# Kernel tuning notes

Measured on AMD Instinct MI355X. Metric: run time of the kernel, lower is better.

Reference implementation:

```python
import jax, jax.numpy as jnp
import numpy as np

G = 8        # GroupNorm groups
PAD = 2      # kernel 5 -> same padding
TOPK = 2
TEMP = 1.0
EPS_GN = 1e-5

def conv1d(x, w):
    # x: (B,C,T), w: (Cout,Cin,K)
    return jax.lax.conv_general_dilated(x, w, (1,), [(PAD, PAD)],
                                        dimension_numbers=('NCH', 'OIH', 'NCH'))

def group_norm(x, g, b):
    B, C, T = x.shape
    xg = x.reshape(B, G, C // G, T)
    m = xg.mean((2, 3), keepdims=True)
    v = xg.var((2, 3), keepdims=True)
    xn = ((xg - m) * jax.lax.rsqrt(v + EPS_GN)).reshape(B, C, T)
    return xn * g[None, :, None] + b[None, :, None]

def gelu(x):
    return jax.nn.gelu(x, approximate=False)  # torch nn.GELU default (erf)

def layer_norm(x, g, b):
    m = x.mean(-1, keepdims=True)
    v = x.var(-1, keepdims=True)
    return (x - m) * jax.lax.rsqrt(v + EPS_GN) * g + b

def cnn_block(x, W1, g1, b1, W2, g2, b2, W3, g3, b3):
    # conv -> GN -> GELU, 3 layers, channel doubling (dropout=eval identity)
    h = gelu(group_norm(conv1d(x, W1), g1, b1))
    h = gelu(group_norm(conv1d(h, W2), g2, b2))
    h = gelu(group_norm(conv1d(h, W3), g3, b3))
    return h

def setup_inputs() -> dict:
    key = jax.random.key(0)
    ks = iter(jax.random.split(key, 64))
    def rn(shape, s):
        return jax.random.normal(next(ks), shape, jnp.float32) * s
    B, Cin, T = 64, 16, 512
    E, c1, c2, c3 = 8, 64, 128, 256
    Hrt, Drt, H, NC = 128, 64, 256, 10
    d = {}
    d['x'] = jax.random.normal(next(ks), (B, Cin, T), jnp.float32)
    # stacked expert CNN params (E leading axis)
    d['eW1'] = rn((E, c1, Cin, 5), 0.1); d['eg1'] = jnp.ones((E, c1)); d['eb1'] = jnp.zeros((E, c1))
    d['eW2'] = rn((E, c2, c1, 5), 0.05); d['eg2'] = jnp.ones((E, c2)); d['eb2'] = jnp.zeros((E, c2))
    d['eW3'] = rn((E, c3, c2, 5), 0.04); d['eg3'] = jnp.ones((E, c3)); d['eb3'] = jnp.zeros((E, c3))
    # shared (always-on) expert CNN
    d['sW1'] = rn((c1, Cin, 5), 0.1); d['sg1'] = jnp.ones((c1,)); d['sb1'] = jnp.zeros((c1,))
    d['sW2'] = rn((c2, c1, 5), 0.05); d['sg2'] = jnp.ones((c2,)); d['sb2'] = jnp.zeros((c2,))
    d['sW3'] = rn((c3, c2, 5), 0.04); d['sg3'] = jnp.ones((c3,)); d['sb3'] = jnp.zeros((c3,))
    # ContextProjRouter: conv front-end -> GAP -> 2-layer MLP
    d['rW'] = rn((Hrt, Cin, 5), 0.1); d['rg'] = jnp.ones((Hrt,)); d['rb'] = jnp.zeros((Hrt,))
    d['rm1W'] = rn((Hrt, Hrt), 0.08); d['rm1b'] = jnp.zeros((Hrt,))
    d['rlng'] = jnp.ones((Hrt,)); d['rlnb'] = jnp.zeros((Hrt,))
    d['rm2W'] = rn((Hrt, Drt), 0.08); d['rm2b'] = jnp.zeros((Drt,))
    # MOEGate linear
    d['gW'] = rn((Drt, E), 0.1); d['gb'] = jnp.zeros((E,))
    # LSTM (single layer, torch gate order i,f,g,o; forget bias = 1)
    d['W_ih'] = rn((c3, 4 * H), 0.04)
    d['W_hh'] = rn((H, 4 * H), 0.04)
    bl = np.zeros(4 * H, np.float32); bl[H:2 * H] = 1.0
    d['b_lstm'] = jnp.asarray(bl)
    # classifier head
    d['Wc'] = rn((H, NC), 0.05); d['bc'] = jnp.zeros((NC,))
    return d

def reference(x, eW1, eg1, eb1, eW2, eg2, eb2, eW3, eg3, eb3,
              sW1, sg1, sb1, sW2, sg2, sb2, sW3, sg3, sb3,
              rW, rg, rb, rm1W, rm1b, rlng, rlnb, rm2W, rm2b,
              gW, gb, W_ih, W_hh, b_lstm, Wc, bc):
    B = x.shape[0]
    # --- expert branches (vmapped over E) -> (E,B,256,T) ---
    expert_out = jax.vmap(
        lambda W1, g1, b1, W2, g2, b2, W3, g3, b3:
            cnn_block(x, W1, g1, b1, W2, g2, b2, W3, g3, b3)
    )(eW1, eg1, eb1, eW2, eg2, eb2, eW3, eg3, eb3)
    # --- shared expert (always on) ---
    shared = cnn_block(x, sW1, sg1, sb1, sW2, sg2, sb2, sW3, sg3, sb3)
    # --- router: conv -> GN -> GELU -> GAP -> MLP ---
    rh = gelu(group_norm(conv1d(x, rW), rg, rb)).mean(-1)      # (B,128)
    r = gelu(layer_norm(rh @ rm1W + rm1b, rlng, rlnb)) @ rm2W + rm2b  # (B,64)
    # --- MOEGate: softmax -> top-k mask -> renormalize ---
    w_soft = jax.nn.softmax((r @ gW + gb) / TEMP, axis=-1)     # (B,E)
    _, idx = jax.lax.top_k(w_soft, TOPK)                       # (B,K)
    mask = jnp.zeros_like(w_soft).at[jnp.arange(B)[:, None], idx].set(1.0)
    w_hard = w_soft * mask
    w_hard = w_hard / (w_hard.sum(-1, keepdims=True) + 1e-9)
    # --- weighted expert mixture + shared ---
    h = shared + jnp.einsum('be,ebct->bct', w_hard, expert_out)  # (B,256,T)
    # --- LSTM over time, take last hidden state ---
    H = W_hh.shape[0]
    seq = h.transpose(2, 0, 1)  # (T,B,256)
    def step(carry, xt):
        hh, cc = carry
        gates = xt @ W_ih + hh @ W_hh + b_lstm
        i, f, g, o = jnp.split(gates, 4, axis=-1)
        cc = jax.nn.sigmoid(f) * cc + jax.nn.sigmoid(i) * jnp.tanh(g)
        hh = jax.nn.sigmoid(o) * jnp.tanh(cc)
        return (hh, cc), None
    init = (jnp.zeros((B, H), x.dtype), jnp.zeros((B, H), x.dtype))
    (hT, _), _ = jax.lax.scan(step, init, seq)
    return hT @ Wc + bc  # (B,num_classes)
```

## Files before the change

kernel.cpp:

```cpp
#include <hip/hip_runtime.h>
#include <cstdint>
#include <cstddef>


#define DEVI __device__ __forceinline__

typedef _Float16 f16;
typedef _Float16 f16x8 __attribute__((ext_vector_type(8)));
typedef _Float16 f16x2 __attribute__((ext_vector_type(2)));
typedef float    f32x4 __attribute__((ext_vector_type(4)));
typedef unsigned int u32;
typedef unsigned short u16;

static constexpr int B   = 64;
static constexpr int T   = 512;
static constexpr int NC  = 10;
static constexpr int NU  = 192;

constexpr size_t SZ_WS1 = (size_t)5*64*32*2;
constexpr size_t SZ_WS2 = (size_t)5*128*64*2;
constexpr size_t SZ_WS3 = (size_t)5*256*128*2;
constexpr size_t SZ_WE1 = 8*SZ_WS1;
constexpr size_t SZ_WE2 = 8*SZ_WS2;
constexpr size_t SZ_WE3 = 8*SZ_WS3;
constexpr size_t SZ_WR  = (size_t)5*128*32*2;
constexpr size_t SZ_WIH = (size_t)1024*256*2;
constexpr size_t SZ_WHH = (size_t)128*1024*4;
constexpr size_t SZ_ACT0 = (size_t)B*T*32*2;
constexpr size_t SZ_RACT = (size_t)B*T*128*2;
constexpr size_t SZ_AMIX = (size_t)B*T*256*2;
constexpr size_t SZ_CONV = (size_t)NU*T*256*2;
constexpr size_t SZ_A1   = (size_t)NU*T*64*2;
constexpr size_t SZ_A2   = (size_t)NU*T*128*2;
constexpr size_t SZ_U    = (size_t)B*T*1024*2;
constexpr size_t SZ_STAT = (size_t)NU*8*2*4;
constexpr size_t SZ_STATR= (size_t)B*8*2*4;
constexpr size_t SZ_RH   = (size_t)B*128*4;
constexpr size_t SZ_EIDX = (size_t)B*2*4;
constexpr size_t SZ_SWT  = (size_t)B*2*4;
constexpr size_t SZ_HT   = (size_t)B*256*4;

constexpr size_t OFF_WS1  = 0;
constexpr size_t OFF_WS2  = OFF_WS1 + SZ_WS1;
constexpr size_t OFF_WS3  = OFF_WS2 + SZ_WS2;
constexpr size_t OFF_WE1  = OFF_WS3 + SZ_WS3;
constexpr size_t OFF_WE2  = OFF_WE1 + SZ_WE1;
constexpr size_t OFF_WE3  = OFF_WE2 + SZ_WE2;
constexpr size_t OFF_WR   = OFF_WE3 + SZ_WE3;
constexpr size_t OFF_WIH  = OFF_WR  + SZ_WR;
constexpr size_t OFF_WHH  = OFF_WIH + SZ_WIH;
constexpr size_t OFF_ACT0 = OFF_WHH + SZ_WHH;
constexpr size_t OFF_RACT = OFF_ACT0 + SZ_ACT0;
constexpr size_t OFF_AMIX = OFF_RACT + SZ_RACT;
constexpr size_t OFF_CONV = OFF_AMIX + SZ_AMIX;
constexpr size_t OFF_A1   = OFF_CONV + SZ_CONV;
constexpr size_t OFF_A2   = OFF_A1 + SZ_A1;
constexpr size_t OFF_U    = OFF_CONV;
constexpr size_t OFF_STAT = OFF_A2 + SZ_A2;
constexpr size_t OFF_STATR= OFF_STAT + SZ_STAT;
constexpr size_t OFF_RH   = OFF_STATR + SZ_STATR;
constexpr size_t OFF_EIDX = OFF_RH + SZ_RH;
constexpr size_t OFF_SWT  = OFF_EIDX + SZ_EIDX;
constexpr size_t OFF_HT   = OFF_SWT + SZ_SWT;
constexpr size_t WS_TOTAL = OFF_HT + SZ_HT;

static_assert(SZ_U <= SZ_CONV + SZ_A1 + SZ_A2, "U alias overflow");

DEVI float geluf(float x){ return 0.5f*x*(1.f + erff(x*0.70710678118654752f)); }
DEVI float fsig(float x){ return 1.f/(1.f + __expf(-x)); }
DEVI float ftanh(float x){ float e = __expf(-2.f*x); return (1.f-e)/(1.f+e); }

DEVI void fill_convw(f16* dst, const float* src, int COUT, int CI, int CIP, int idx){
  int s  = idx / (COUT*CIP);
  int r  = idx - s*(COUT*CIP);
  int co = r / CIP;
  int ci = r - co*CIP;
  float v = (ci < CI) ? src[((size_t)co*CI + ci)*5 + s] : 0.f;
  dst[idx] = (f16)v;
}

__global__ __launch_bounds__(256) void k_prep_w(
    const float* eW1, const float* eW2, const float* eW3,
    const float* sW1, const float* sW2, const float* sW3, const float* rW,
    const float* Wih, const float* Whh, char* ws)
{
  int i = blockIdx.x*256 + threadIdx.x;
  if (i < 10240){ fill_convw((f16*)(ws+OFF_WS1), sW1, 64, 16, 32, i); return; } i -= 10240;
  if (i < 40960){ fill_convw((f16*)(ws+OFF_WS2), sW2, 128, 64, 64, i); return; } i -= 40960;
  if (i < 163840){ fill_convw((f16*)(ws+OFF_WS3), sW3, 256, 128, 128, i); return; } i -= 163840;
  if (i < 81920){ int e=i/10240, r=i-e*10240;
    fill_convw((f16*)(ws+OFF_WE1)+ (size_t)e*10240, eW1 + (size_t)e*64*16*5, 64, 16, 32, r); return; } i -= 81920;
  if (i < 327680){ int e=i/40960, r=i-e*40960;
    fill_convw((f16*)(ws+OFF_WE2)+ (size_t)e*40960, eW2 + (size_t)e*128*64*5, 128, 64, 64, r); return; } i -= 327680;
  if (i < 1310720){ int e=i/163840, r=i-e*163840;
    fill_convw((f16*)(ws+OFF_WE3)+ (size_t)e*163840, eW3 + (size_t)e*163840, 256, 128, 128, r); return; } i -= 1310720;
  if (i < 20480){ fill_convw((f16*)(ws+OFF_WR), rW, 128, 16, 32, i); return; } i -= 20480;
  if (i < 262144){
    int j = i >> 8, k = i & 255;
    ((f16*)(ws+OFF_WIH))[i] = (f16)Wih[(size_t)k*1024 + j]; return; } i -= 262144;
  if (i < 131072){
    int i2 = i >> 10, j = i & 1023;
    f16 a = (f16)Whh[(size_t)(2*i2)*1024 + j];
    f16 b = (f16)Whh[(size_t)(2*i2+1)*1024 + j];
    u32 u = (u32)__builtin_bit_cast(unsigned short, a)
          | ((u32)__builtin_bit_cast(unsigned short, b) << 16);
    ((u32*)(ws+OFF_WHH))[i] = u; return; }
}

__global__ __launch_bounds__(256) void k_prep_x(const float* __restrict__ x, char* ws){
  int idx = blockIdx.x*256 + threadIdx.x;
  if (idx >= B*T*32) return;
  int b = idx/(T*32); int r = idx - b*(T*32); int t = r >> 5; int c = r & 31;
  f16 v = (c < 16) ? (f16)x[((size_t)b*16 + c)*T + t] : (f16)0.f;
  ((f16*)(ws+OFF_ACT0))[idx] = v;
}

template<int CIN, int NSHIFT>
__global__ __launch_bounds__(256) void k_conv(
    const f16* __restrict__ act, long actUnitStride,
    const f16* __restrict__ wtS, const f16* __restrict__ wtE, long wtEStride,
    const int* __restrict__ eidx,
    f16* __restrict__ outp, const float* __restrict__ bias, int COUT)
{
  int u = blockIdx.z;
  int s = u >> 6, b = u & 63;
  const f16* wt = wtS;
  if (eidx && s < 2) wt = wtE + (size_t)eidx[b*2+s]*wtEStride;
  const f16* abase = act + (actUnitStride ? (size_t)u*actUnitStride
                                          : (size_t)b*T*CIN);
  f16* obase = outp + (size_t)u*T*COUT;

  int t0 = blockIdx.x << 6;
  int n0 = blockIdx.y << 6;
  int tid  = threadIdx.x;
  int wave = tid >> 6, lane = tid & 63;
  int lr = lane & 15, lk = lane >> 4;

  f32x4 acc[4];
  #pragma unroll
  for (int nf=0; nf<4; ++nf) acc[nf] = f32x4{0.f,0.f,0.f,0.f};

  int trow = t0 + wave*16 + lr;

  #pragma unroll
  for (int sh=0; sh<NSHIFT; ++sh){
    int tg = (NSHIFT==5) ? (trow + sh - 2) : trow;
    bool valid = (unsigned)tg < (unsigned)T;
    const f16* arow = abase + (long)tg*CIN + lk*8;
    #pragma unroll
    for (int c0=0; c0<CIN; c0+=32){
      f16x8 af = {(f16)0,(f16)0,(f16)0,(f16)0,(f16)0,(f16)0,(f16)0,(f16)0};
      if (valid) af = *(const f16x8*)(arow + c0);
      #pragma unroll
      for (int nf=0; nf<4; ++nf){
        int col = n0 + nf*16 + lr;
        f16x8 bf = *(const f16x8*)(wt + ((size_t)sh*COUT + col)*CIN + c0 + lk*8);
        acc[nf] = __builtin_amdgcn_mfma_f32_16x16x32_f16(af, bf, acc[nf], 0, 0, 0);
      }
    }
  }

  #pragma unroll
  for (int nf=0; nf<4; ++nf){
    int col = n0 + nf*16 + lr;
    float bv = bias ? bias[col] : 0.f;
    #pragma unroll
    for (int r=0; r<4; ++r){
      int trw = t0 + wave*16 + lk*4 + r;
      obase[(size_t)trw*COUT + col] = (f16)(acc[nf][r] + bv);
    }
  }
}

template<int CPG>
__global__ __launch_bounds__(256) void k_gnstats(
    const f16* __restrict__ xin, float* __restrict__ stats)
{
  constexpr int C = CPG*8;
  constexpr int V = CPG/8;
  int u = blockIdx.x >> 3, g = blockIdx.x & 7;
  const f16* base = xin + (size_t)u*T*C + g*CPG;
  float sum = 0.f, ss = 0.f;
  for (int i = threadIdx.x; i < T*V; i += 256){
    int t = i / V, v = i - (i/V)*V;
    f16x8 xv = *(const f16x8*)(base + (size_t)t*C + v*8);
    #pragma unroll
    for (int k=0;k<8;++k){ float f = (float)xv[k]; sum += f; ss += f*f; }
  }
  #pragma unroll
  for (int off=32; off; off>>=1){ sum += __shfl_down(sum, off); ss += __shfl_down(ss, off); }
  __shared__ float rs[8];
  int wave = threadIdx.x >> 6, lane = threadIdx.x & 63;
  if (lane == 0){ rs[wave] = sum; rs[4+wave] = ss; }
  __syncthreads();
  if (threadIdx.x == 0){
    float S = rs[0]+rs[1]+rs[2]+rs[3], Q = rs[4]+rs[5]+rs[6]+rs[7];
    constexpr float N = (float)(CPG*T);
    float m = S/N;
    float var = Q/N - m*m;
    stats[(u*8+g)*2]   = m;
    stats[(u*8+g)*2+1] = rsqrtf(var + 1e-5f);
  }
}

template<int CPG>
__global__ __launch_bounds__(256) void k_gnapply(
    const f16* __restrict__ xin, const float* __restrict__ stats,
    const float* __restrict__ gS, const float* __restrict__ bS,
    const float* __restrict__ gE, const float* __restrict__ bE,
    const int* __restrict__ eidx, f16* __restrict__ outp, int total8)
{
  constexpr int C = CPG*8;
  int idx = blockIdx.x*256 + threadIdx.x;
  if (idx >= total8) return;
  size_t base = (size_t)idx*8;
  int u = (int)(base / ((size_t)T*C));
  int s = u >> 6, b = u & 63;
  const float* gamma = gS; const float* beta = bS;
  if (eidx && s < 2){ int e = eidx[b*2+s]; gamma = gE + e*C; beta = bE + e*C; }
  int c0 = (int)(base % C);
  int g  = c0 / CPG;
  float m  = stats[(u*8+g)*2];
  float rstd = stats[(u*8+g)*2+1];
  f16x8 xv = *(const f16x8*)(xin + base);
  f16x8 h8;
  #pragma unroll
  for (int k=0; k<8; ++k){
    float xn = ((float)xv[k]-m)*rstd*gamma[c0+k] + beta[c0+k];
    h8[k] = (f16)geluf(xn);
  }
  *(f16x8*)(outp + base) = h8;
}

__global__ __launch_bounds__(256) void k_gnmix(
    const f16* __restrict__ conv, const float* __restrict__ stats,
    const float* __restrict__ sg, const float* __restrict__ sb,
    const float* __restrict__ eg, const float* __restrict__ eb,
    const int* __restrict__ eidx, const float* __restrict__ swt,
    f16* __restrict__ amix)
{
  size_t base = ((size_t)blockIdx.x*256 + threadIdx.x)*8;
  if (base >= (size_t)B*T*256) return;
  int b = (int)(base / ((size_t)T*256));
  size_t rem = base - (size_t)b*T*256;
  int c0 = (int)(rem & 255);
  int g  = c0 >> 5;
  float o[8] = {0.f,0.f,0.f,0.f,0.f,0.f,0.f,0.f};
  #pragma unroll
  for (int s=0; s<3; ++s){
    int u = s*64 + b;
    float w; const float *gamma, *beta;
    if (s < 2){ int e = eidx[b*2+s]; w = swt[b*2+s]; gamma = eg + e*256; beta = eb + e*256; }
    else      { w = 1.f; gamma = sg; beta = sb; }
    float m = stats[(u*8+g)*2], rstd = stats[(u*8+g)*2+1];
    f16x8 xv = *(const f16x8*)(conv + (size_t)u*T*256 + rem);
    #pragma unroll
    for (int k=0; k<8; ++k){
      float xn = ((float)xv[k]-m)*rstd*gamma[c0+k] + beta[c0+k];
      o[k] += w*geluf(xn);
    }
  }
  f16x8 h8;
  #pragma unroll
  for (int k=0; k<8; ++k) h8[k] = (f16)o[k];
  *(f16x8*)(amix + base) = h8;
}

__global__ __launch_bounds__(512) void k_gap(const f16* __restrict__ ract,
                                             float* __restrict__ rh){
  int b = blockIdx.x;
  int c = threadIdx.x & 127, st = threadIdx.x >> 7;
  const f16* p = ract + (size_t)b*T*128 + c;
  float s = 0.f;
  for (int t = st; t < T; t += 4) s += (float)p[(size_t)t*128];
  __shared__ float acc[512];
  acc[threadIdx.x] = s;
  __syncthreads();
  if (st == 0) rh[b*128 + c] = (acc[c] + acc[128+c] + acc[256+c] + acc[384+c]) * (1.f/(float)T);
}

__global__ __launch_bounds__(128) void k_router(
    const float* __restrict__ rh,
    const float* __restrict__ m1W, const float* __restrict__ m1b,
    const float* __restrict__ lng, const float* __restrict__ lnb,
    const float* __restrict__ m2W, const float* __restrict__ m2b,
    const float* __restrict__ gW,  const float* __restrict__ gb,
    int* __restrict__ eidx, float* __restrict__ swt)
{
  int b = blockIdx.x, j = threadIdx.x;
  __shared__ float sbuf[128];
  __shared__ float red[4];
  __shared__ float z2[64];
  sbuf[j] = rh[b*128 + j];
  __syncthreads();
  float acc = m1b[j];
  for (int k=0; k<128; ++k) acc += sbuf[k]*m1W[k*128 + j];
  float s1 = acc, s2 = acc*acc;
  #pragma unroll
  for (int off=32; off; off>>=1){ s1 += __shfl_down(s1, off); s2 += __shfl_down(s2, off); }
  int wid = j >> 6, lane = j & 63;
  if (lane == 0){ red[wid] = s1; red[2+wid] = s2; }
  __syncthreads();
  float S = red[0]+red[1], Q = red[2]+red[3];
  float m = S*(1.f/128.f), var = Q*(1.f/128.f) - m*m;
  float xn = (acc - m)*rsqrtf(var + 1e-5f)*lng[j] + lnb[j];
  float ge = geluf(xn);
  __syncthreads();
  sbuf[j] = ge;
  __syncthreads();
  if (j < 64){
    float a = m2b[j];
    for (int k=0; k<128; ++k) a += sbuf[k]*m2W[k*64 + j];
    z2[j] = a;
  }
  __syncthreads();
  if (j == 0){
    float lg[8];
    for (int e=0; e<8; ++e){
      float a = gb[e];
      for (int k=0; k<64; ++k) a += z2[k]*gW[k*8 + e];
      lg[e] = a;
    }
    float mx = lg[0];
    for (int e=1; e<8; ++e) mx = fmaxf(mx, lg[e]);
    float p[8], sum = 0.f;
    for (int e=0; e<8; ++e){ p[e] = __expf(lg[e]-mx); sum += p[e]; }
    float inv = 1.f/sum;
    for (int e=0; e<8; ++e) p[e] *= inv;
    int i1 = 0;
    for (int e=1; e<8; ++e) if (p[e] > p[i1]) i1 = e;
    int i2 = -1;
    for (int e=0; e<8; ++e){ if (e==i1) continue; if (i2 < 0 || p[e] > p[i2]) i2 = e; }
    float s = p[i1] + p[i2] + 1e-9f;
    eidx[b*2]   = i1;  swt[b*2]   = p[i1]/s;
    eidx[b*2+1] = i2;  swt[b*2+1] = p[i2]/s;
  }
}

constexpr int PV5 = 100;
constexpr int PLQ = 7;

DEVI float dot2acc(u32 wu, u32 hu, float acc){
#if __has_builtin(__builtin_amdgcn_fdot2)
  return __builtin_amdgcn_fdot2(__builtin_bit_cast(f16x2, wu),
                                __builtin_bit_cast(f16x2, hu), acc, false);
#else
  f16x2 a = __builtin_bit_cast(f16x2, wu), b = __builtin_bit_cast(f16x2, hu);
  return acc + (float)a.x*(float)b.x + (float)a.y*(float)b.y;
#endif
}

__global__ __attribute__((amdgpu_flat_work_group_size(512,512), amdgpu_waves_per_eu(2,2)))
void k_lstm(const u32* __restrict__ whh, const f16* __restrict__ U,
            float* __restrict__ hTout)
{
  int b = blockIdx.x, j = threadIdx.x;
  int d = j & 255, half = j >> 8;
  int colA = half*256 + d;
  int colB = 512 + colA;

  __shared__ u32 wl[PLQ*4*1024];
  __shared__ __align__(16) u32 hbuf[2][128];
  __shared__ float gbF[256], gbO[256];

  u32 wA[PV5], wB[PV5];
  #pragma unroll
  for (int i=0; i<PV5; ++i){
    wA[i] = whh[(size_t)i*1024 + colA];
    wB[i] = whh[(size_t)i*1024 + colB];
  }
  for (int idx = j; idx < PLQ*4*1024; idx += 512){
    int p = idx >> 10, c = idx & 1023;
    wl[idx] = whh[(size_t)(PV5+p)*1024 + c];
  }
  if (j < 128) hbuf[0][j] = 0u;

  float cst = 0.f, hst = 0.f;
  const f16* Ub = U + (size_t)b*T*1024;
  float uA = (float)Ub[colA], uB = (float)Ub[colB];
  __syncthreads();

  int cur = 0;
  for (int t=0; t<T; ++t){
    float aA = uA, aB = uB;
    if (t+1 < T){
      const f16* un = Ub + (size_t)(t+1)*1024;
      uA = (float)un[colA]; uB = (float)un[colB];
    }
    const uint4* hp4 = (const uint4*)hbuf[cur];
    #pragma unroll
    for (int q=0; q<PV5/4; ++q){
      uint4 hq = hp4[q];
      aA = dot2acc(wA[4*q+0], hq.x, aA); aB = dot2acc(wB[4*q+0], hq.x, aB);
      aA = dot2acc(wA[4*q+1], hq.y, aA); aB = dot2acc(wB[4*q+1], hq.y, aB);
      aA = dot2acc(wA[4*q+2], hq.z, aA); aB = dot2acc(wB[4*q+2], hq.z, aB);
      aA = dot2acc(wA[4*q+3], hq.w, aA); aB = dot2acc(wB[4*q+3], hq.w, aB);
    }
    #pragma unroll
    for (int k=0; k<PLQ; ++k){
      uint4 hq = hp4[PV5/4 + k];
      u32 a0 = wl[(4*k+0)*1024 + colA], b0 = wl[(4*k+0)*1024 + colB];
      u32 a1 = wl[(4*k+1)*1024 + colA], b1 = wl[(4*k+1)*1024 + colB];
      u32 a2 = wl[(4*k+2)*1024 + colA], b2 = wl[(4*k+2)*1024 + colB];
      u32 a3 = wl[(4*k+3)*1024 + colA], b3 = wl[(4*k+3)*1024 + colB];
      aA = dot2acc(a0, hq.x, aA); aB = dot2acc(b0, hq.x, aB);
      aA = dot2acc(a1, hq.y, aA); aB = dot2acc(b1, hq.y, aB);
      aA = dot2acc(a2, hq.z, aA); aB = dot2acc(b2, hq.z, aB);
      aA = dot2acc(a3, hq.w, aA); aB = dot2acc(b3, hq.w, aB);
    }
    if (half){ gbF[d] = aA; gbO[d] = aB; }
    __syncthreads();
    if (!half){
      float gi = aA, gg = aB, gf = gbF[d], go = gbO[d];
      cst = fsig(gf)*cst + fsig(gi)*ftanh(gg);
      hst = fsig(go)*ftanh(cst);
      u16* hn = (u16*)hbuf[cur^1];
      hn[d] = __builtin_bit_cast(u16, (f16)hst);
    }
    __syncthreads();
    cur ^= 1;
  }
  if (!half) hTout[b*256 + d] = hst;
}

__global__ __launch_bounds__(256) void k_head(const float* __restrict__ hT,
    const float* __restrict__ Wc, const float* __restrict__ bc,
    float* __restrict__ out)
{
  int b = blockIdx.x, j = threadIdx.x;
  __shared__ float hs[256];
  hs[j] = hT[b*256 + j];
  __syncthreads();
  if (j < NC){
    float a = bc[j];
    for (int k=0; k<256; ++k) a += hs[k]*Wc[k*NC + j];
    out[b*NC + j] = a;
  }
}

extern "C" void kernel_launch(void* const* d_in, const int* in_sizes, int n_in,
                              void* d_out, int out_size, void* d_ws, size_t ws_size,
                              hipStream_t stream)
{
  if (ws_size < WS_TOTAL) return;

  const float* x    = (const float*)d_in[0];
  const float* eW1  = (const float*)d_in[1];
  const float* eg1  = (const float*)d_in[2];
  const float* eb1  = (const float*)d_in[3];
  const float* eW2  = (const float*)d_in[4];
  const float* eg2  = (const float*)d_in[5];
  const float* eb2  = (const float*)d_in[6];
  const float* eW3  = (const float*)d_in[7];
  const float* eg3  = (const float*)d_in[8];
  const float* eb3  = (const float*)d_in[9];
  const float* sW1  = (const float*)d_in[10];
  const float* sg1  = (const float*)d_in[11];
  const float* sb1  = (const float*)d_in[12];
  const float* sW2  = (const float*)d_in[13];
  const float* sg2  = (const float*)d_in[14];
  const float* sb2  = (const float*)d_in[15];
  const float* sW3  = (const float*)d_in[16];
  const float* sg3  = (const float*)d_in[17];
  const float* sb3  = (const float*)d_in[18];
  const float* rW   = (const float*)d_in[19];
  const float* rg   = (const float*)d_in[20];
  const float* rb   = (const float*)d_in[21];
  const float* rm1W = (const float*)d_in[22];
  const float* rm1b = (const float*)d_in[23];
  const float* rlng = (const float*)d_in[24];
  const float* rlnb = (const float*)d_in[25];
  const float* rm2W = (const float*)d_in[26];
  const float* rm2b = (const float*)d_in[27];
  const float* gW   = (const float*)d_in[28];
  const float* gb   = (const float*)d_in[29];
  const float* Wih  = (const float*)d_in[30];
  const float* Whh  = (const float*)d_in[31];
  const float* blst = (const float*)d_in[32];
  const float* Wc   = (const float*)d_in[33];
  const float* bc   = (const float*)d_in[34];

  char* ws = (char*)d_ws;
  f16*  ws1   = (f16*)(ws + OFF_WS1);
  f16*  ws2   = (f16*)(ws + OFF_WS2);
  f16*  ws3   = (f16*)(ws + OFF_WS3);
  f16*  we1   = (f16*)(ws + OFF_WE1);
  f16*  we2   = (f16*)(ws + OFF_WE2);
  f16*  we3   = (f16*)(ws + OFF_WE3);
  f16*  wr    = (f16*)(ws + OFF_WR);
  f16*  wih   = (f16*)(ws + OFF_WIH);
  u32*  whh   = (u32*)(ws + OFF_WHH);
  f16*  act0  = (f16*)(ws + OFF_ACT0);
  f16*  ract  = (f16*)(ws + OFF_RACT);
  f16*  amix  = (f16*)(ws + OFF_AMIX);
  f16*  convb = (f16*)(ws + OFF_CONV);
  f16*  a1    = (f16*)(ws + OFF_A1);
  f16*  a2    = (f16*)(ws + OFF_A2);
  f16*  Ubuf  = (f16*)(ws + OFF_U);
  float* stats = (float*)(ws + OFF_STAT);
  float* statsR= (float*)(ws + OFF_STATR);
  float* rh    = (float*)(ws + OFF_RH);
  int*   eidx  = (int*)(ws + OFF_EIDX);
  float* swt   = (float*)(ws + OFF_SWT);
  float* hTb   = (float*)(ws + OFF_HT);

  k_prep_w<<<(2349056 + 255)/256, 256, 0, stream>>>(eW1,eW2,eW3,sW1,sW2,sW3,rW,Wih,Whh,ws);
  k_prep_x<<<(B*T*32 + 255)/256, 256, 0, stream>>>(x, ws);

  k_conv<32,5><<<dim3(8,2,64), 256, 0, stream>>>(act0, 0L, wr, nullptr, 0L, nullptr, convb, nullptr, 128);
  k_gnstats<16><<<64*8, 256, 0, stream>>>(convb, statsR);
  k_gnapply<16><<<2048, 256, 0, stream>>>(convb, statsR, rg, rb, nullptr, nullptr, nullptr, ract, 64*T*128/8);
  k_gap<<<B, 512, 0, stream>>>(ract, rh);
  k_router<<<B, 128, 0, stream>>>(rh, rm1W, rm1b, rlng, rlnb, rm2W, rm2b, gW, gb, eidx, swt);

  k_conv<32,5><<<dim3(8,1,NU), 256, 0, stream>>>(act0, 0L, ws1, we1, (long)(5*64*32), eidx, convb, nullptr, 64);
  k_gnstats<8><<<NU*8, 256, 0, stream>>>(convb, stats);
  k_gnapply<8><<<3072, 256, 0, stream>>>(convb, stats, sg1, sb1, eg1, eb1, eidx, a1, NU*T*64/8);

  k_conv<64,5><<<dim3(8,2,NU), 256, 0, stream>>>(a1, (long)T*64, ws2, we2, (long)(5*128*64), eidx, convb, nullptr, 128);
  k_gnstats<16><<<NU*8, 256, 0, stream>>>(convb, stats);
  k_gnapply<16><<<6144, 256, 0, stream>>>(convb, stats, sg2, sb2, eg2, eb2, eidx, a2, NU*T*128/8);

  k_conv<128,5><<<dim3(8,4,NU), 256, 0, stream>>>(a2, (long)T*128, ws3, we3, (long)(5*256*128), eidx, convb, nullptr, 256);
  k_gnstats<32><<<NU*8, 256, 0, stream>>>(convb, stats);
  k_gnmix<<<4096, 256, 0, stream>>>(convb, stats, sg3, sb3, eg3, eb3, eidx, swt, amix);

  k_conv<256,1><<<dim3(8,16,64), 256, 0, stream>>>(amix, 0L, wih, nullptr, 0L, nullptr, Ubuf, blst, 1024);
  k_lstm<<<B, 512, 0, stream>>>(whh, Ubuf, hTb);
  k_head<<<B, 256, 0, stream>>>(hTb, Wc, bc, (float*)d_out);
}
```

Before: 1.657 ms.

## Fuse conv, GroupNorm stats, apply and GELU into one per-unit layer kernel

Replaces the separate conv, GroupNorm-stats and GroupNorm-apply kernels with a single kernel per layer. Each block computes the full time extent of one unit's conv output into shared memory, reduces the group statistics there, and applies normalisation plus GELU before writing. For the router this also folds global average pooling into the same kernel. This removes the fp16 round trips of the conv output through global memory and several launches. The cost is far fewer blocks (192 or 384 per layer, 64 for the router) and heavy LDS use (up to 128 KB per block), which limits occupancy.

Result: slower. 1.773 ms (+7.0%).

```diff
diff --git a/kernel.cpp b/kernel.cpp
--- a/kernel.cpp
+++ b/kernel.cpp
@@ -115,6 +115,144 @@
   ((f16*)(ws+OFF_ACT0))[idx] = v;
 }
 
+template<int CIN, int COUT_BLK, int CPG, bool GAP>
+__global__ __launch_bounds__(512) void k_layer(
+    const f16* __restrict__ act, long actUnitStride,
+    const f16* __restrict__ wtS, const f16* __restrict__ wtE, long wtEStride,
+    const int* __restrict__ eidx,
+    const float* __restrict__ gS, const float* __restrict__ bS,
+    const float* __restrict__ gE, const float* __restrict__ bE,
+    int COUT_TOTAL,
+    f16* __restrict__ outp, long outUnitStride, int outStride,
+    float* __restrict__ rhOut)
+{
+  constexpr int CH8  = COUT_BLK/8;
+  constexpr int NG   = COUT_BLK/CPG;
+  constexpr int CPW  = CPG/8;
+  constexpr int NPASS = COUT_BLK/64;
+  constexpr int ROWSTEP = 512/CH8;
+  constexpr int ITERS   = T/ROWSTEP;
+
+  int u = blockIdx.x, hf = blockIdx.y;
+  int s_ = u >> 6, b = u & 63;
+  const f16* wt = wtS;
+  const float* gamma = gS; const float* beta = bS;
+  if (eidx && s_ < 2){
+    int e = eidx[b*2 + s_];
+    wt    = wtE + (size_t)e*wtEStride;
+    gamma = gE + (size_t)e*COUT_TOTAL;
+    beta  = bE + (size_t)e*COUT_TOTAL;
+  }
+  gamma += hf*COUT_BLK; beta += hf*COUT_BLK;
+  const f16* abase = act + (actUnitStride ? (size_t)u*actUnitStride
+                                          : (size_t)b*T*CIN);
+  int wcol0 = hf*COUT_BLK;
+
+  __shared__ f16 tile[T*COUT_BLK];
+  __shared__ float cpart[8][CH8][2];
+  __shared__ float mr[NG][2];
+  __shared__ float gcol[GAP ? 8 : 1][GAP ? CH8 : 1][8];
+
+  int tid = threadIdx.x;
+  int wave = tid >> 6, lane = tid & 63;
+  int lr = lane & 15, lk = lane >> 4;
+
+  for (int mt = wave; mt < 32; mt += 8){
+    int trow = mt*16 + lr;
+    #pragma unroll
+    for (int np = 0; np < NPASS; ++np){
+      f32x4 acc[4];
+      #pragma unroll
+      for (int nf=0; nf<4; ++nf) acc[nf] = f32x4{0.f,0.f,0.f,0.f};
+      #pragma unroll
+      for (int sh = 0; sh < 5; ++sh){
+        int tg = trow + sh - 2;
+        bool valid = (unsigned)tg < (unsigned)T;
+        const f16* arow = abase + (long)tg*CIN + lk*8;
+        #pragma unroll
+        for (int c0=0; c0<CIN; c0+=32){
+          f16x8 af = {(f16)0,(f16)0,(f16)0,(f16)0,(f16)0,(f16)0,(f16)0,(f16)0};
+          if (valid) af = *(const f16x8*)(arow + c0);
+          #pragma unroll
+          for (int nf=0; nf<4; ++nf){
+            int col = wcol0 + np*64 + nf*16 + lr;
+            f16x8 bf = *(const f16x8*)(wt + ((size_t)sh*COUT_TOTAL + col)*CIN + c0 + lk*8);
+            acc[nf] = __builtin_amdgcn_mfma_f32_16x16x32_f16(af, bf, acc[nf], 0, 0, 0);
+          }
+        }
+      }
+      #pragma unroll
+      for (int nf=0; nf<4; ++nf)
+        #pragma unroll
+        for (int r=0; r<4; ++r)
+          tile[(size_t)(mt*16 + lk*4 + r)*COUT_BLK + np*64 + nf*16 + lr] = (f16)acc[nf][r];
+    }
+  }
+  __syncthreads();
+
+  int chunk = tid & (CH8-1);
+  int row0  = tid / CH8;
+  float sum = 0.f, ss = 0.f;
+  #pragma unroll
+  for (int k=0; k<ITERS; ++k){
+    int row = row0 + k*ROWSTEP;
+    f16x8 xv = *(const f16x8*)(tile + (size_t)row*COUT_BLK + chunk*8);
+    #pragma unroll
+    for (int e=0;e<8;++e){ float f = (float)xv[e]; sum += f; ss += f*f; }
+  }
+  #pragma unroll
+  for (int mk=CH8; mk<=32; mk<<=1){ sum += __shfl_xor(sum, mk); ss += __shfl_xor(ss, mk); }
+  if (lane < CH8){ cpart[wave][lane][0] = sum; cpart[wave][lane][1] = ss; }
+  __syncthreads();
+  if (tid < NG){
+    float S = 0.f, Q = 0.f;
+    for (int w2=0; w2<8; ++w2)
+      for (int cc=0; cc<CPW; ++cc){ S += cpart[w2][tid*CPW+cc][0]; Q += cpart[w2][tid*CPW+cc][1]; }
+    constexpr float N = (float)(CPG*T);
+    float m = S/N, var = Q/N - m*m;
+    mr[tid][0] = m; mr[tid][1] = rsqrtf(var + 1e-5f);
+  }
+  __syncthreads();
+
+  int g = chunk / CPW;
+  float m = mr[g][0], rstd = mr[g][1];
+  float gm[8], bt[8];
+  #pragma unroll
+  for (int e=0;e<8;++e){ gm[e] = gamma[chunk*8+e]; bt[e] = beta[chunk*8+e]; }
+  float cs[8] = {0.f,0.f,0.f,0.f,0.f,0.f,0.f,0.f};
+  f16* obase = outp ? (outp + (size_t)u*outUnitStride + hf*COUT_BLK) : nullptr;
+  #pragma unroll
+  for (int k=0; k<ITERS; ++k){
+    int row = row0 + k*ROWSTEP;
+    f16x8 xv = *(const f16x8*)(tile + (size_t)row*COUT_BLK + chunk*8);
+    f16x8 h8;
+    #pragma unroll
+    for (int e=0;e<8;++e){
+      float xn = ((float)xv[e]-m)*rstd*gm[e] + bt[e];
+      float o = geluf(xn);
+      if constexpr (GAP) cs[e] += o; else h8[e] = (f16)o;
+    }
+    if constexpr (!GAP)
+      *(f16x8*)(obase + (size_t)row*outStride + chunk*8) = h8;
+  }
+  if constexpr (GAP){
+    #pragma unroll
+    for (int mk=CH8; mk<=32; mk<<=1)
+      #pragma unroll
+      for (int e=0;e<8;++e) cs[e] += __shfl_xor(cs[e], mk);
+    if (lane < CH8)
+      #pragma unroll
+      for (int e=0;e<8;++e) gcol[wave][lane][e] = cs[e];
+    __syncthreads();
+    if (tid < COUT_BLK){
+      int c = tid >> 3, e = tid & 7;
+      float tot = 0.f;
+      for (int w2=0; w2<8; ++w2) tot += gcol[w2][c][e];
+      rhOut[b*128 + tid] = tot * (1.f/(float)T);
+    }
+  }
+}
+
 template<int CIN, int NSHIFT>
 __global__ __launch_bounds__(256) void k_conv(
     const f16* __restrict__ act, long actUnitStride,
@@ -172,111 +310,23 @@
   }
 }
 
-template<int CPG>
-__global__ __launch_bounds__(256) void k_gnstats(
-    const f16* __restrict__ xin, float* __restrict__ stats)
-{
-  constexpr int C = CPG*8;
-  constexpr int V = CPG/8;
-  int u = blockIdx.x >> 3, g = blockIdx.x & 7;
-  const f16* base = xin + (size_t)u*T*C + g*CPG;
-  float sum = 0.f, ss = 0.f;
-  for (int i = threadIdx.x; i < T*V; i += 256){
-    int t = i / V, v = i - (i/V)*V;
-    f16x8 xv = *(const f16x8*)(base + (size_t)t*C + v*8);
-    #pragma unroll
-    for (int k=0;k<8;++k){ float f = (float)xv[k]; sum += f; ss += f*f; }
-  }
-  #pragma unroll
-  for (int off=32; off; off>>=1){ sum += __shfl_down(sum, off); ss += __shfl_down(ss, off); }
-  __shared__ float rs[8];
-  int wave = threadIdx.x >> 6, lane = threadIdx.x & 63;
-  if (lane == 0){ rs[wave] = sum; rs[4+wave] = ss; }
-  __syncthreads();
-  if (threadIdx.x == 0){
-    float S = rs[0]+rs[1]+rs[2]+rs[3], Q = rs[4]+rs[5]+rs[6]+rs[7];
-    constexpr float N = (float)(CPG*T);
-    float m = S/N;
-    float var = Q/N - m*m;
-    stats[(u*8+g)*2]   = m;
-    stats[(u*8+g)*2+1] = rsqrtf(var + 1e-5f);
-  }
-}
-
-template<int CPG>
-__global__ __launch_bounds__(256) void k_gnapply(
-    const f16* __restrict__ xin, const float* __restrict__ stats,
-    const float* __restrict__ gS, const float* __restrict__ bS,
-    const float* __restrict__ gE, const float* __restrict__ bE,
-    const int* __restrict__ eidx, f16* __restrict__ outp, int total8)
-{
-  constexpr int C = CPG*8;
-  int idx = blockIdx.x*256 + threadIdx.x;
-  if (idx >= total8) return;
-  size_t base = (size_t)idx*8;
-  int u = (int)(base / ((size_t)T*C));
-  int s = u >> 6, b = u & 63;
-  const float* gamma = gS; const float* beta = bS;
-  if (eidx && s < 2){ int e = eidx[b*2+s]; gamma = gE + e*C; beta = bE + e*C; }
-  int c0 = (int)(base % C);
-  int g  = c0 / CPG;
-  float m  = stats[(u*8+g)*2];
-  float rstd = stats[(u*8+g)*2+1];
-  f16x8 xv = *(const f16x8*)(xin + base);
-  f16x8 h8;
-  #pragma unroll
-  for (int k=0; k<8; ++k){
-    float xn = ((float)xv[k]-m)*rstd*gamma[c0+k] + beta[c0+k];
-    h8[k] = (f16)geluf(xn);
-  }
-  *(f16x8*)(outp + base) = h8;
-}
-
-__global__ __launch_bounds__(256) void k_gnmix(
-    const f16* __restrict__ conv, const float* __restrict__ stats,
-    const float* __restrict__ sg, const float* __restrict__ sb,
-    const float* __restrict__ eg, const float* __restrict__ eb,
-    const int* __restrict__ eidx, const float* __restrict__ swt,
+__global__ __launch_bounds__(256) void k_mix(
+    const f16* __restrict__ conv, const float* __restrict__ swt,
     f16* __restrict__ amix)
 {
   size_t base = ((size_t)blockIdx.x*256 + threadIdx.x)*8;
   if (base >= (size_t)B*T*256) return;
   int b = (int)(base / ((size_t)T*256));
   size_t rem = base - (size_t)b*T*256;
-  int c0 = (int)(rem & 255);
-  int g  = c0 >> 5;
-  float o[8] = {0.f,0.f,0.f,0.f,0.f,0.f,0.f,0.f};
-  #pragma unroll
-  for (int s=0; s<3; ++s){
-    int u = s*64 + b;
-    float w; const float *gamma, *beta;
-    if (s < 2){ int e = eidx[b*2+s]; w = swt[b*2+s]; gamma = eg + e*256; beta = eb + e*256; }
-    else      { w = 1.f; gamma = sg; beta = sb; }
-    float m = stats[(u*8+g)*2], rstd = stats[(u*8+g)*2+1];
-    f16x8 xv = *(const f16x8*)(conv + (size_t)u*T*256 + rem);
-    #pragma unroll
-    for (int k=0; k<8; ++k){
-      float xn = ((float)xv[k]-m)*rstd*gamma[c0+k] + beta[c0+k];
-      o[k] += w*geluf(xn);
-    }
-  }
+  float w0 = swt[b*2], w1 = swt[b*2+1];
+  f16x8 x0 = *(const f16x8*)(conv + ((size_t)(b))*T*256 + rem);
+  f16x8 x1 = *(const f16x8*)(conv + ((size_t)(64+b))*T*256 + rem);
+  f16x8 x2 = *(const f16x8*)(conv + ((size_t)(128+b))*T*256 + rem);
   f16x8 h8;
   #pragma unroll
-  for (int k=0; k<8; ++k) h8[k] = (f16)o[k];
+  for (int e=0; e<8; ++e)
+    h8[e] = (f16)(w0*(float)x0[e] + w1*(float)x1[e] + (float)x2[e]);
   *(f16x8*)(amix + base) = h8;
-}
-
-__global__ __launch_bounds__(512) void k_gap(const f16* __restrict__ ract,
-                                             float* __restrict__ rh){
-  int b = blockIdx.x;
-  int c = threadIdx.x & 127, st = threadIdx.x >> 7;
-  const f16* p = ract + (size_t)b*T*128 + c;
-  float s = 0.f;
-  for (int t = st; t < T; t += 4) s += (float)p[(size_t)t*128];
-  __shared__ float acc[512];
-  acc[threadIdx.x] = s;
-  __syncthreads();
-  if (st == 0) rh[b*128 + c] = (acc[c] + acc[128+c] + acc[256+c] + acc[384+c]) * (1.f/(float)T);
 }
 
 __global__ __launch_bounds__(128) void k_router(
@@ -491,14 +541,11 @@
   f16*  wih   = (f16*)(ws + OFF_WIH);
   u32*  whh   = (u32*)(ws + OFF_WHH);
   f16*  act0  = (f16*)(ws + OFF_ACT0);
-  f16*  ract  = (f16*)(ws + OFF_RACT);
   f16*  amix  = (f16*)(ws + OFF_AMIX);
   f16*  convb = (f16*)(ws + OFF_CONV);
   f16*  a1    = (f16*)(ws + OFF_A1);
   f16*  a2    = (f16*)(ws + OFF_A2);
   f16*  Ubuf  = (f16*)(ws + OFF_U);
-  float* stats = (float*)(ws + OFF_STAT);
-  float* statsR= (float*)(ws + OFF_STATR);
   float* rh    = (float*)(ws + OFF_RH);
   int*   eidx  = (int*)(ws + OFF_EIDX);
   float* swt   = (float*)(ws + OFF_SWT);
@@ -507,23 +554,22 @@
   k_prep_w<<<(2349056 + 255)/256, 256, 0, stream>>>(eW1,eW2,eW3,sW1,sW2,sW3,rW,Wih,Whh,ws);
   k_prep_x<<<(B*T*32 + 255)/256, 256, 0, stream>>>(x, ws);
 
-  k_conv<32,5><<<dim3(8,2,64), 256, 0, stream>>>(act0, 0L, wr, nullptr, 0L, nullptr, convb, nullptr, 128);
-  k_gnstats<16><<<64*8, 256, 0, stream>>>(convb, statsR);
-  k_gnapply<16><<<2048, 256, 0, stream>>>(convb, statsR, rg, rb, nullptr, nullptr, nullptr, ract, 64*T*128/8);
-  k_gap<<<B, 512, 0, stream>>>(ract, rh);
+  k_layer<32,128,16,true><<<dim3(64,1), 512, 0, stream>>>(
+      act0, 0L, wr, nullptr, 0L, nullptr, rg, rb, nullptr, nullptr, 128,
+      nullptr, 0L, 0, rh);
   k_router<<<B, 128, 0, stream>>>(rh, rm1W, rm1b, rlng, rlnb, rm2W, rm2b, gW, gb, eidx, swt);
 
-  k_conv<32,5><<<dim3(8,1,NU), 256, 0, stream>>>(act0, 0L, ws1, we1, (long)(5*64*32), eidx, convb, nullptr, 64);
-  k_gnstats<8><<<NU*8, 256, 0, stream>>>(convb, stats);
-  k_gnapply<8><<<3072, 256, 0, stream>>>(convb, stats, sg1, sb1, eg1, eb1, eidx, a1, NU*T*64/8);
-
-  k_conv<64,5><<<dim3(8,2,NU), 256, 0, stream>>>(a1, (long)T*64, ws2, we2, (long)(5*128*64), eidx, convb, nullptr, 128);
-  k_gnstats<16><<<NU*8, 256, 0, stream>>>(convb, stats);
-  k_gnapply<16><<<6144, 256, 0, stream>>>(convb, stats, sg2, sb2, eg2, eb2, eidx, a2, NU*T*128/8);
-
-  k_conv<128,5><<<dim3(8,4,NU), 256, 0, stream>>>(a2, (long)T*128, ws3, we3, (long)(5*256*128), eidx, convb, nullptr, 256);
-  k_gnstats<32><<<NU*8, 256, 0, stream>>>(convb, stats);
-  k_gnmix<<<4096, 256, 0, stream>>>(convb, stats, sg3, sb3, eg3, eb3, eidx, swt, amix);
+  k_layer<32,64,8,false><<<dim3(NU,1), 512, 0, stream>>>(
+      act0, 0L, ws1, we1, (long)(5*64*32), eidx, sg1, sb1, eg1, eb1, 64,
+      a1, (long)T*64, 64, nullptr);
+  k_layer<64,128,16,false><<<dim3(NU,1), 512, 0, stream>>>(
+      a1, (long)T*64, ws2, we2, (long)(5*128*64), eidx, sg2, sb2, eg2, eb2, 128,
+      a2, (long)T*128, 128, nullptr);
+  k_layer<128,128,32,false><<<dim3(NU,2), 512, 0, stream>>>(
+      a2, (long)T*128, ws3, we3, (long)(5*256*128), eidx, sg3, sb3, eg3, eb3, 256,
+      convb, (long)T*256, 256, nullptr);
+
+  k_mix<<<(B*T*256/8 + 255)/256, 256, 0, stream>>>(convb, swt, amix);
 
   k_conv<256,1><<<dim3(8,16,64), 256, 0, stream>>>(amix, 0L, wih, nullptr, 0L, nullptr, Ubuf, blst, 1024);
   k_lstm<<<B, 512, 0, stream>>>(whh, Ubuf, hTb);
```
